# Performance work log

Hardware: AMD Instinct MI355X
Metric: run time of the kernel (lower is better)

Reference implementation:

```python
import jax, jax.numpy as jnp
import numpy as np

B, N, NINP, NFEAT, H = 4096, 4096, 64, 32, 4


def setup_inputs() -> dict:
    key = jax.random.key(0)
    ks = jax.random.split(key, 8)
    s_in = 1.0 / np.sqrt(NINP)
    s_att = 1.0 / np.sqrt(2 * NFEAT)
    return {
        "X": jax.random.normal(ks[0], (B, NINP), jnp.float32),
        "G": jax.random.normal(ks[1], (N, NINP), jnp.float32),
        "A": jax.random.uniform(ks[2], (B, N), jnp.float32),  # additive mask
        "W": jax.random.uniform(ks[3], (H, NINP, NFEAT), jnp.float32, -s_in, s_in),
        "b": jax.random.uniform(ks[4], (H, NFEAT), jnp.float32, -s_in, s_in),
        "a_src": jax.random.uniform(ks[5], (H, NFEAT), jnp.float32, -s_att, s_att),
        "a_dst": jax.random.uniform(ks[6], (H, NFEAT), jnp.float32, -s_att, s_att),
        "att_b": jax.random.uniform(ks[7], (H,), jnp.float32, -s_att, s_att),
    }


def reference(X, G, A, W, b, a_src, a_dst, att_b):
    # Per-head linear transforms (all heads batched via einsum)
    WX = jnp.einsum("bi,hif->bhf", X, W) + b            # (B, H, F)
    WG = jnp.einsum("ni,hif->nhf", G, W) + b            # (N, H, F)
    # Decomposed concat-attention: a^T [WX_b ; WG_n] = a_src.WX_b + a_dst.WG_n
    s_src = jnp.einsum("bhf,hf->bh", WX, a_src)         # (B, H)
    s_dst = jnp.einsum("nhf,hf->nh", WG, a_dst)         # (N, H)
    e = s_src[:, :, None] + s_dst.T[None, :, :] + att_b[None, :, None]  # (B,H,N)
    att = jax.nn.softmax(e - A[:, None, :], axis=-1)    # adjacency-masked softmax
    # Dropout(0.5) is identity in eval mode (deterministic reference).
    out = jnp.einsum("bhn,nhf->bhf", att, WG)           # weighted aggregation
    out = jax.nn.relu(out)                              # activation before concat
    return out.reshape(out.shape[0], -1)                # (B, H*F) concat heads
```

## Files before the change

### kernel.cpp

```cpp
#include <hip/hip_runtime.h>
#include <stdint.h>

#define N_TOK 4096
#define D_IN  64
#define NF    32
#define NH    4
#define OUTW  (NH * NF)
#define NT    8
#define CHUNK 128
#define BT    64

typedef float        f32x4  __attribute__((ext_vector_type(4)));
typedef unsigned int uint4v __attribute__((ext_vector_type(4)));
typedef __bf16       bf16x8 __attribute__((ext_vector_type(8)));

union Frag { uint4v u; bf16x8 v; };

static __device__ __forceinline__ unsigned short f2bf_rne(float x) {
  unsigned u = __float_as_uint(x);
  u += 0x7fffu + ((u >> 16) & 1u);
  return (unsigned short)(u >> 16);
}

__global__ __launch_bounds__(128) void prep_kernel(
    const float* __restrict__ G, const float* __restrict__ W,
    const float* __restrict__ bias, const float* __restrict__ a_dst,
    unsigned short* __restrict__ PB) {
  __shared__ float gs[NT * D_IN];
  const int tid = threadIdx.x;
  const int n0  = blockIdx.x * NT;
  {
    const float4* src = (const float4*)(G + (size_t)n0 * D_IN);
    float4* dst = (float4*)gs;
    dst[tid] = src[tid];
  }
  __syncthreads();
  const int h = tid >> 5, f = tid & 31;
  float acc[NT];
  const float bb = bias[h * NF + f];
#pragma unroll
  for (int k = 0; k < NT; ++k) acc[k] = bb;
#pragma unroll
  for (int i = 0; i < D_IN; ++i) {
    const float wv = W[(h * D_IN + i) * NF + f];
#pragma unroll
    for (int k = 0; k < NT; ++k) acc[k] = fmaf(gs[k * D_IN + i], wv, acc[k]);
  }
  const float ad = a_dst[h * NF + f];
  float ev[NT];
#pragma unroll
  for (int k = 0; k < NT; ++k) {
    float s = acc[k] * ad;
    s += __shfl_xor(s, 1);  s += __shfl_xor(s, 2);  s += __shfl_xor(s, 4);
    s += __shfl_xor(s, 8);  s += __shfl_xor(s, 16);
    ev[k] = __expf(s);
  }
  const int t   = n0 >> 5;
  const int gq  = (n0 >> 3) & 3;
  const int set = (h << 1) | (f >> 4);
  const int col = f & 15;
  union { uint4 u4; unsigned short us[8]; } pk;
#pragma unroll
  for (int k = 0; k < NT; ++k) pk.us[k] = f2bf_rne(acc[k] * ev[k]);
  *(uint4*)(PB + (size_t)((((t * 9 + set) << 6) + (gq << 4) + col)) * 8) = pk.u4;
  if (f == 0) {
    union { uint4 u4; unsigned short us[8]; } pe;
#pragma unroll
    for (int k = 0; k < NT; ++k) pe.us[k] = f2bf_rne(ev[k]);
    *(uint4*)(PB + (size_t)((((t * 9 + 8) << 6) + (gq << 4) + h)) * 8) = pe.u4;
  }
  if (h == 0 && f >= 4 && f < 16) {
    uint4 z; z.x = 0u; z.y = 0u; z.z = 0u; z.w = 0u;
    *(uint4*)(PB + (size_t)((((t * 9 + 8) << 6) + (gq << 4) + f)) * 8) = z;
  }
}

template <int NS>
__global__ __launch_bounds__(512) void attn_kernel(
    const float* __restrict__ A, const unsigned short* __restrict__ PB,
    float* __restrict__ op, float* __restrict__ dp, float* __restrict__ out) {
  constexpr int NHALF  = N_TOK / NS;
  constexpr int NIT    = NHALF / CHUNK;
  constexpr int RINGSZ = BT * CHUNK * 2;
  __shared__ __align__(16) unsigned short ring[3 * BT * CHUNK];
  __shared__ float denLds[BT * NH];
  char* ringb = (char*)ring;

  const int tid  = threadIdx.x;
  const int lane = tid & 63;
  const int w    = tid >> 6;
  const int bid  = blockIdx.x;
  const int s    = bid & (NS - 1);
  const int b0   = (bid / NS) * BT;

  const int srow = tid >> 3, tp = tid & 7;
  const float* abase = A + (size_t)(b0 + srow) * N_TOK + s * NHALF + tp * 16;
  const int wb0 = srow * 256 + (((tp * 2    ) ^ (srow & 15)) << 4);
  const int wb1 = srow * 256 + (((tp * 2 + 1) ^ (srow & 15)) << 4);

  const int rowm = lane & 15, g = lane >> 4;
  const char* pbb  = (const char*)PB + (size_t)s * (NHALF / 32) * 9216;
  const char* pown = pbb + (((w << 6) + lane) << 4);
  const char* pden = pbb + (((8 << 6) + lane) << 4);

  f32x4 acc0  = {0.f, 0.f, 0.f, 0.f}, acc1  = {0.f, 0.f, 0.f, 0.f};
  f32x4 acc2  = {0.f, 0.f, 0.f, 0.f}, acc3  = {0.f, 0.f, 0.f, 0.f};
  f32x4 accd0 = {0.f, 0.f, 0.f, 0.f}, accd1 = {0.f, 0.f, 0.f, 0.f};
  f32x4 accd2 = {0.f, 0.f, 0.f, 0.f}, accd3 = {0.f, 0.f, 0.f, 0.f};
  f32x4 aXa, aXb, aXc, aXd, aYa, aYb, aYc, aYd;
  Frag bo0, bo1, bo2, bo3, bd0, bd1, bd2, bd3;
  Frag co0, co1, co2, co3, cd0, cd1, cd2, cd3;
  int mR = 0, mW = 1;

#define LOADA4(d0, d1, d2, d3, cc) do {                                        \
    const float* ap_ = abase + (size_t)(cc) * CHUNK;                           \
    asm volatile("global_load_dwordx4 %0, %1, off"                            \
                 : "=v"(d0) : "v"(ap_) : "memory");                            \
    asm volatile("global_load_dwordx4 %0, %1, off"                            \
                 : "=v"(d1) : "v"(ap_ + 4) : "memory");                        \
    asm volatile("global_load_dwordx4 %0, %1, off"                            \
                 : "=v"(d2) : "v"(ap_ + 8) : "memory");                        \
    asm volatile("global_load_dwordx4 %0, %1, off"                            \
                 : "=v"(d3) : "v"(ap_ + 12) : "memory");                       \
  } while (0)
#define LOADBO(fr, cc, kk)                                                     \
  asm volatile("global_load_dwordx4 %0, %1, off"                              \
               : "=v"(fr.u)                                                    \
               : "v"(pown + (size_t)((cc) * 4 + (kk)) * 9216) : "memory")
#define LOADBD(fr, cc, kk)                                                     \
  asm volatile("global_load_dwordx4 %0, %1, off"                              \
               : "=v"(fr.u)                                                    \
               : "v"(pden + (size_t)((cc) * 4 + (kk)) * 9216) : "memory")

#define EXPP(AV0, AV1, AV2, AV3, mw) do {                                      \
    float x0 = __expf(-AV0[0]), x1 = __expf(-AV0[1]);                          \
    float x2 = __expf(-AV0[2]), x3 = __expf(-AV0[3]);                          \
    float x4 = __expf(-AV1[0]), x5 = __expf(-AV1[1]);                          \
    float x6 = __expf(-AV1[2]), x7 = __expf(-AV1[3]);                          \
    float y0 = __expf(-AV2[0]), y1 = __expf(-AV2[1]);                          \
    float y2 = __expf(-AV2[2]), y3 = __expf(-AV2[3]);                          \
    float y4 = __expf(-AV3[0]), y5 = __expf(-AV3[1]);                          \
    float y6 = __expf(-AV3[2]), y7 = __expf(-AV3[3]);                          \
    uint4v t_, u_;                                                             \
    t_[0] = __builtin_amdgcn_perm(__float_as_uint(x1), __float_as_uint(x0), 0x07060302u); \
    t_[1] = __builtin_amdgcn_perm(__float_as_uint(x3), __float_as_uint(x2), 0x07060302u); \
    t_[2] = __builtin_amdgcn_perm(__float_as_uint(x5), __float_as_uint(x4), 0x07060302u); \
    t_[3] = __builtin_amdgcn_perm(__float_as_uint(x7), __float_as_uint(x6), 0x07060302u); \
    u_[0] = __builtin_amdgcn_perm(__float_as_uint(y1), __float_as_uint(y0), 0x07060302u); \
    u_[1] = __builtin_amdgcn_perm(__float_as_uint(y3), __float_as_uint(y2), 0x07060302u); \
    u_[2] = __builtin_amdgcn_perm(__float_as_uint(y5), __float_as_uint(y4), 0x07060302u); \
    u_[3] = __builtin_amdgcn_perm(__float_as_uint(y7), __float_as_uint(y6), 0x07060302u); \
    char* rb_ = ringb + (mw) * RINGSZ;                                         \
    *(uint4v*)(rb_ + wb0) = t_;                                                \
    *(uint4v*)(rb_ + wb1) = u_;                                                \
  } while (0)

#define AF(rg, kk)                                                             \
  (*(const bf16x8*)(ringb + mR * RINGSZ + ((rg) * 16 + rowm) * 256 +           \
                    ((((kk) * 4 + g) ^ rowm) << 4)))
#define MQD(ACC, ACCD, rg, kk, FB, FD) do {                                    \
    Frag af_; af_.v = AF(rg, kk);                                              \
    ACC  = __builtin_amdgcn_mfma_f32_16x16x32_bf16(af_.v, FB.v, ACC,  0, 0, 0);\
    ACCD = __builtin_amdgcn_mfma_f32_16x16x32_bf16(af_.v, FD.v, ACCD, 0, 0, 0);\
  } while (0)
#define MQO(ACC, rg, kk, FB) do {                                              \
    Frag af_; af_.v = AF(rg, kk);                                              \
    ACC = __builtin_amdgcn_mfma_f32_16x16x32_bf16(af_.v, FB.v, ACC, 0, 0, 0);  \
  } while (0)

#define ITERD(cc, AC0, AC1, AC2, AC3, AN0, AN1, AN2, AN3,                      \
              CO0, CO1, CO2, CO3, CD0, CD1, CD2, CD3,                          \
              NO0, NO1, NO2, NO3, ND0, ND1, ND2, ND3) do {                     \
    { const int cb_ = ((cc) + 1 < NIT) ? (cc) + 1 : NIT - 1;                   \
      LOADBO(NO0, cb_, 0); LOADBO(NO1, cb_, 1);                                \
      LOADBO(NO2, cb_, 2); LOADBO(NO3, cb_, 3);                                \
      LOADBD(ND0, cb_, 0); LOADBD(ND1, cb_, 1);                                \
      LOADBD(ND2, cb_, 2); LOADBD(ND3, cb_, 3); }                              \
    { const int ca_ = ((cc) + 2 < NIT) ? (cc) + 2 : NIT - 1;                   \
      LOADA4(AN0, AN1, AN2, AN3, ca_); }                                       \
    asm volatile("s_waitcnt vmcnt(12)" ::: "memory");                          \
    __builtin_amdgcn_sched_barrier(0);                                         \
    EXPP(AC0, AC1, AC2, AC3, mW);                                              \
    asm volatile("s_waitcnt lgkmcnt(0)" ::: "memory");                         \
    __builtin_amdgcn_sched_barrier(0);                                         \
    __builtin_amdgcn_s_barrier();                                              \
    MQD(acc0, accd0, 0, 0, CO0, CD0); MQD(acc1, accd1, 1, 0, CO0, CD0);        \
    MQD(acc2, accd2, 2, 0, CO0, CD0); MQD(acc3, accd3, 3, 0, CO0, CD0);        \
    MQD(acc0, accd0, 0, 1, CO1, CD1); MQD(acc1, accd1, 1, 1, CO1, CD1);        \
    MQD(acc2, accd2, 2, 1, CO1, CD1); MQD(acc3, accd3, 3, 1, CO1, CD1);        \
    MQD(acc0, accd0, 0, 2, CO2, CD2); MQD(acc1, accd1, 1, 2, CO2, CD2);        \
    MQD(acc2, accd2, 2, 2, CO2, CD2); MQD(acc3, accd3, 3, 2, CO2, CD2);        \
    MQD(acc0, accd0, 0, 3, CO3, CD3); MQD(acc1, accd1, 1, 3, CO3, CD3);        \
    MQD(acc2, accd2, 2, 3, CO3, CD3); MQD(acc3, accd3, 3, 3, CO3, CD3);        \
    mR = mW; mW = (mW + 1 == 3) ? 0 : mW + 1;                                  \
  } while (0)
#define ITERO(cc, AC0, AC1, AC2, AC3, AN0, AN1, AN2, AN3,                      \
              CO0, CO1, CO2, CO3, NO0, NO1, NO2, NO3) do {                     \
    { const int cb_ = ((cc) + 1 < NIT) ? (cc) + 1 : NIT - 1;                   \
      LOADBO(NO0, cb_, 0); LOADBO(NO1, cb_, 1);                                \
      LOADBO(NO2, cb_, 2); LOADBO(NO3, cb_, 3); }                              \
    { const int ca_ = ((cc) + 2 < NIT) ? (cc) + 2 : NIT - 1;                   \
      LOADA4(AN0, AN1, AN2, AN3, ca_); }                                       \
    asm volatile("s_waitcnt vmcnt(8)" ::: "memory");                           \
    __builtin_amdgcn_sched_barrier(0);                                         \
    EXPP(AC0, AC1, AC2, AC3, mW);                                              \
    asm volatile("s_waitcnt lgkmcnt(0)" ::: "memory");                         \
    __builtin_amdgcn_sched_barrier(0);                                         \
    __builtin_amdgcn_s_barrier();                                              \
    MQO(acc0, 0, 0, CO0); MQO(acc1, 1, 0, CO0);                                \
    MQO(acc2, 2, 0, CO0); MQO(acc3, 3, 0, CO0);                                \
    MQO(acc0, 0, 1, CO1); MQO(acc1, 1, 1, CO1);                                \
    MQO(acc2, 2, 1, CO1); MQO(acc3, 3, 1, CO1);                                \
    MQO(acc0, 0, 2, CO2); MQO(acc1, 1, 2, CO2);                                \
    MQO(acc2, 2, 2, CO2); MQO(acc3, 3, 2, CO2);                                \
    MQO(acc0, 0, 3, CO3); MQO(acc1, 1, 3, CO3);                                \
    MQO(acc2, 2, 3, CO3); MQO(acc3, 3, 3, CO3);                                \
    mR = mW; mW = (mW + 1 == 3) ? 0 : mW + 1;                                  \
  } while (0)

  if (w == 0) {
    LOADA4(aXa, aXb, aXc, aXd, 0);
    LOADBO(bo0, 0, 0); LOADBO(bo1, 0, 1); LOADBO(bo2, 0, 2); LOADBO(bo3, 0, 3);
    LOADBD(bd0, 0, 0); LOADBD(bd1, 0, 1); LOADBD(bd2, 0, 2); LOADBD(bd3, 0, 3);
    LOADA4(aYa, aYb, aYc, aYd, 1);
    asm volatile("s_waitcnt vmcnt(12)" ::: "memory");
    __builtin_amdgcn_sched_barrier(0);
    EXPP(aXa, aXb, aXc, aXd, 0);
#pragma unroll 1
    for (int i = 0; i < NIT; i += 2) {
      ITERD(i,     aYa, aYb, aYc, aYd, aXa, aXb, aXc, aXd,
                   bo0, bo1, bo2, bo3, bd0, bd1, bd2, bd3,
                   co0, co1, co2, co3, cd0, cd1, cd2, cd3);
      ITERD(i + 1, aXa, aXb, aXc, aXd, aYa, aYb, aYc, aYd,
                   co0, co1, co2, co3, cd0, cd1, cd2, cd3,
                   bo0, bo1, bo2, bo3, bd0, bd1, bd2, bd3);
    }
  } else {
    LOADA4(aXa, aXb, aXc, aXd, 0);
    LOADBO(bo0, 0, 0); LOADBO(bo1, 0, 1); LOADBO(bo2, 0, 2); LOADBO(bo3, 0, 3);
    LOADA4(aYa, aYb, aYc, aYd, 1);
    asm volatile("s_waitcnt vmcnt(8)" ::: "memory");
    __builtin_amdgcn_sched_barrier(0);
    EXPP(aXa, aXb, aXc, aXd, 0);
#pragma unroll 1
    for (int i = 0; i < NIT; i += 2) {
      ITERO(i,     aYa, aYb, aYc, aYd, aXa, aXb, aXc, aXd,
                   bo0, bo1, bo2, bo3, co0, co1, co2, co3);
      ITERO(i + 1, aXa, aXb, aXc, aXd, aYa, aYb, aYc, aYd,
                   co0, co1, co2, co3, bo0, bo1, bo2, bo3);
    }
  }

  asm volatile("s_waitcnt vmcnt(0)" ::: "memory");
  __builtin_amdgcn_sched_barrier(0);

  if (NS == 1) {
    if (w == 0 && rowm < NH) {
#pragma unroll
      for (int r = 0; r < 4; ++r) {
        denLds[(     g * 4 + r) * NH + rowm] = accd0[r];
        denLds[(16 + g * 4 + r) * NH + rowm] = accd1[r];
        denLds[(32 + g * 4 + r) * NH + rowm] = accd2[r];
        denLds[(48 + g * 4 + r) * NH + rowm] = accd3[r];
      }
    }
    __syncthreads();
    const int hh = w >> 1;
#pragma unroll
    for (int r = 0; r < 4; ++r) {
      const int rr = g * 4 + r;
      float o;
      o = acc0[r] / denLds[(     rr) * NH + hh];
      out[(size_t)(b0 +      rr) * OUTW + w * 16 + rowm] = o > 0.f ? o : 0.f;
      o = acc1[r] / denLds[(16 + rr) * NH + hh];
      out[(size_t)(b0 + 16 + rr) * OUTW + w * 16 + rowm] = o > 0.f ? o : 0.f;
      o = acc2[r] / denLds[(32 + rr) * NH + hh];
      out[(size_t)(b0 + 32 + rr) * OUTW + w * 16 + rowm] = o > 0.f ? o : 0.f;
      o = acc3[r] / denLds[(48 + rr) * NH + hh];
      out[(size_t)(b0 + 48 + rr) * OUTW + w * 16 + rowm] = o > 0.f ? o : 0.f;
    }
  } else {
    float* ob = op + (size_t)s * (N_TOK * OUTW) + (size_t)b0 * OUTW + w * 16 + rowm;
#pragma unroll
    for (int r = 0; r < 4; ++r) {
      const int rr = g * 4 + r;
      ob[(size_t)(     rr) * OUTW] = acc0[r];
      ob[(size_t)(16 + rr) * OUTW] = acc1[r];
      ob[(size_t)(32 + rr) * OUTW] = acc2[r];
      ob[(size_t)(48 + rr) * OUTW] = acc3[r];
    }
    if (w == 0 && rowm < NH) {
#pragma unroll
      for (int r = 0; r < 4; ++r) {
        const int rr = g * 4 + r;
        dp[((size_t)s * N_TOK + b0 +      rr) * NH + rowm] = accd0[r];
        dp[((size_t)s * N_TOK + b0 + 16 + rr) * NH + rowm] = accd1[r];
        dp[((size_t)s * N_TOK + b0 + 32 + rr) * NH + rowm] = accd2[r];
        dp[((size_t)s * N_TOK + b0 + 48 + rr) * NH + rowm] = accd3[r];
      }
    }
  }
#undef LOADA4
#undef LOADBO
#undef LOADBD
#undef EXPP
#undef AF
#undef MQD
#undef MQO
#undef ITERD
#undef ITERO
}

__global__ __launch_bounds__(256) void comb_kernel(
    const float* __restrict__ op, const float* __restrict__ dp,
    float* __restrict__ out, int NS) {
  const int idx4 = blockIdx.x * 256 + threadIdx.x;
  const int eb = idx4 >> 5;
  const int h  = ((idx4 << 2) & 127) >> 5;
  float4 o; o.x = 0.f; o.y = 0.f; o.z = 0.f; o.w = 0.f;
  float d = 0.f;
  for (int s2 = 0; s2 < NS; ++s2) {
    float4 vv = *(const float4*)(op + (size_t)s2 * (N_TOK * OUTW) + (size_t)idx4 * 4);
    o.x += vv.x; o.y += vv.y; o.z += vv.z; o.w += vv.w;
    d += dp[((size_t)s2 * N_TOK + eb) * NH + h];
  }
  const float r = 1.f / d;
  float4 res;
  res.x = fmaxf(o.x * r, 0.f);
  res.y = fmaxf(o.y * r, 0.f);
  res.z = fmaxf(o.z * r, 0.f);
  res.w = fmaxf(o.w * r, 0.f);
  *(float4*)(out + (size_t)idx4 * 4) = res;
}

extern "C" void kernel_launch(void* const* d_in, const int* in_sizes, int n_in,
                              void* d_out, int out_size, void* d_ws, size_t ws_size,
                              hipStream_t stream) {
  const float* G     = (const float*)d_in[1];
  const float* A     = (const float*)d_in[2];
  const float* W     = (const float*)d_in[3];
  const float* bias  = (const float*)d_in[4];
  const float* a_dst = (const float*)d_in[6];

  char* ws = (char*)d_ws;
  const size_t PBsz = (size_t)128 * 9 * 1024;
  const size_t per_split = (size_t)N_TOK * OUTW * 4 + (size_t)N_TOK * NH * 4;

  unsigned short* PB = (unsigned short*)ws;
  float* op = (float*)(ws + PBsz);
  float* outp = (float*)d_out;

  prep_kernel<<<N_TOK / NT, 128, 0, stream>>>(G, W, bias, a_dst, PB);
  if (ws_size >= PBsz + 4 * per_split) {
    float* dp = (float*)(ws + PBsz + 4 * (size_t)N_TOK * OUTW * 4);
    attn_kernel<4><<<(N_TOK / BT) * 4, 512, 0, stream>>>(A, PB, op, dp, nullptr);
    comb_kernel<<<(N_TOK * OUTW / 4) / 256, 256, 0, stream>>>(op, dp, outp, 4);
  } else if (ws_size >= PBsz + 2 * per_split) {
    float* dp = (float*)(ws + PBsz + 2 * (size_t)N_TOK * OUTW * 4);
    attn_kernel<2><<<(N_TOK / BT) * 2, 512, 0, stream>>>(A, PB, op, dp, nullptr);
    comb_kernel<<<(N_TOK * OUTW / 4) / 256, 256, 0, stream>>>(op, dp, outp, 2);
  } else {
    attn_kernel<1><<<N_TOK / BT, 512, 0, stream>>>(A, PB, nullptr, nullptr, outp);
  }
}
```

Before: 32.49 us.

## Add 8-way key split and load denominator B fragments just-in-time

Adds an 8-way split of the key dimension when the workspace is large enough, launching twice as many attention blocks and combining eight partial results afterwards. Wave 0's denominator fragments are no longer double-buffered one chunk ahead; they are loaded at the start of each iteration and waited on just before the MFMAs. This frees registers and adds parallelism for the 64-block-per-split grid, at the cost of extra partial-result traffic in the combine step and less latency hiding for the denominator loads.

```diff
diff --git a/kernel.cpp b/kernel.cpp
--- a/kernel.cpp
+++ b/kernel.cpp
@@ -108,8 +108,9 @@
   f32x4 accd0 = {0.f, 0.f, 0.f, 0.f}, accd1 = {0.f, 0.f, 0.f, 0.f};
   f32x4 accd2 = {0.f, 0.f, 0.f, 0.f}, accd3 = {0.f, 0.f, 0.f, 0.f};
   f32x4 aXa, aXb, aXc, aXd, aYa, aYb, aYc, aYd;
-  Frag bo0, bo1, bo2, bo3, bd0, bd1, bd2, bd3;
-  Frag co0, co1, co2, co3, cd0, cd1, cd2, cd3;
+  Frag bo0, bo1, bo2, bo3;
+  Frag co0, co1, co2, co3;
+  Frag bd0, bd1, bd2, bd3;
   int mR = 0, mW = 1;
 
 #define LOADA4(d0, d1, d2, d3, cc) do {                                        \
@@ -169,13 +170,12 @@
   } while (0)
 
 #define ITERD(cc, AC0, AC1, AC2, AC3, AN0, AN1, AN2, AN3,                      \
-              CO0, CO1, CO2, CO3, CD0, CD1, CD2, CD3,                          \
-              NO0, NO1, NO2, NO3, ND0, ND1, ND2, ND3) do {                     \
+              CO0, CO1, CO2, CO3, NO0, NO1, NO2, NO3) do {                     \
+    LOADBD(bd0, cc, 0); LOADBD(bd1, cc, 1);                                    \
+    LOADBD(bd2, cc, 2); LOADBD(bd3, cc, 3);                                    \
     { const int cb_ = ((cc) + 1 < NIT) ? (cc) + 1 : NIT - 1;                   \
       LOADBO(NO0, cb_, 0); LOADBO(NO1, cb_, 1);                                \
-      LOADBO(NO2, cb_, 2); LOADBO(NO3, cb_, 3);                                \
-      LOADBD(ND0, cb_, 0); LOADBD(ND1, cb_, 1);                                \
-      LOADBD(ND2, cb_, 2); LOADBD(ND3, cb_, 3); }                              \
+      LOADBO(NO2, cb_, 2); LOADBO(NO3, cb_, 3); }                              \
     { const int ca_ = ((cc) + 2 < NIT) ? (cc) + 2 : NIT - 1;                   \
       LOADA4(AN0, AN1, AN2, AN3, ca_); }                                       \
     asm volatile("s_waitcnt vmcnt(12)" ::: "memory");                          \
@@ -184,14 +184,16 @@
     asm volatile("s_waitcnt lgkmcnt(0)" ::: "memory");                         \
     __builtin_amdgcn_sched_barrier(0);                                         \
     __builtin_amdgcn_s_barrier();                                              \
-    MQD(acc0, accd0, 0, 0, CO0, CD0); MQD(acc1, accd1, 1, 0, CO0, CD0);        \
-    MQD(acc2, accd2, 2, 0, CO0, CD0); MQD(acc3, accd3, 3, 0, CO0, CD0);        \
-    MQD(acc0, accd0, 0, 1, CO1, CD1); MQD(acc1, accd1, 1, 1, CO1, CD1);        \
-    MQD(acc2, accd2, 2, 1, CO1, CD1); MQD(acc3, accd3, 3, 1, CO1, CD1);        \
-    MQD(acc0, accd0, 0, 2, CO2, CD2); MQD(acc1, accd1, 1, 2, CO2, CD2);        \
-    MQD(acc2, accd2, 2, 2, CO2, CD2); MQD(acc3, accd3, 3, 2, CO2, CD2);        \
-    MQD(acc0, accd0, 0, 3, CO3, CD3); MQD(acc1, accd1, 1, 3, CO3, CD3);        \
-    MQD(acc2, accd2, 2, 3, CO3, CD3); MQD(acc3, accd3, 3, 3, CO3, CD3);        \
+    asm volatile("s_waitcnt vmcnt(8)" ::: "memory");                           \
+    __builtin_amdgcn_sched_barrier(0);                                         \
+    MQD(acc0, accd0, 0, 0, CO0, bd0); MQD(acc1, accd1, 1, 0, CO0, bd0);        \
+    MQD(acc2, accd2, 2, 0, CO0, bd0); MQD(acc3, accd3, 3, 0, CO0, bd0);        \
+    MQD(acc0, accd0, 0, 1, CO1, bd1); MQD(acc1, accd1, 1, 1, CO1, bd1);        \
+    MQD(acc2, accd2, 2, 1, CO1, bd1); MQD(acc3, accd3, 3, 1, CO1, bd1);        \
+    MQD(acc0, accd0, 0, 2, CO2, bd2); MQD(acc1, accd1, 1, 2, CO2, bd2);        \
+    MQD(acc2, accd2, 2, 2, CO2, bd2); MQD(acc3, accd3, 3, 2, CO2, bd2);        \
+    MQD(acc0, accd0, 0, 3, CO3, bd3); MQD(acc1, accd1, 1, 3, CO3, bd3);        \
+    MQD(acc2, accd2, 2, 3, CO3, bd3); MQD(acc3, accd3, 3, 3, CO3, bd3);        \
     mR = mW; mW = (mW + 1 == 3) ? 0 : mW + 1;                                  \
   } while (0)
 #define ITERO(cc, AC0, AC1, AC2, AC3, AN0, AN1, AN2, AN3,                      \
@@ -221,19 +223,16 @@
   if (w == 0) {
     LOADA4(aXa, aXb, aXc, aXd, 0);
     LOADBO(bo0, 0, 0); LOADBO(bo1, 0, 1); LOADBO(bo2, 0, 2); LOADBO(bo3, 0, 3);
-    LOADBD(bd0, 0, 0); LOADBD(bd1, 0, 1); LOADBD(bd2, 0, 2); LOADBD(bd3, 0, 3);
     LOADA4(aYa, aYb, aYc, aYd, 1);
-    asm volatile("s_waitcnt vmcnt(12)" ::: "memory");
+    asm volatile("s_waitcnt vmcnt(8)" ::: "memory");
     __builtin_amdgcn_sched_barrier(0);
     EXPP(aXa, aXb, aXc, aXd, 0);
 #pragma unroll 1
     for (int i = 0; i < NIT; i += 2) {
       ITERD(i,     aYa, aYb, aYc, aYd, aXa, aXb, aXc, aXd,
-                   bo0, bo1, bo2, bo3, bd0, bd1, bd2, bd3,
-                   co0, co1, co2, co3, cd0, cd1, cd2, cd3);
+                   bo0, bo1, bo2, bo3, co0, co1, co2, co3);
       ITERD(i + 1, aXa, aXb, aXc, aXd, aYa, aYb, aYc, aYd,
-                   co0, co1, co2, co3, cd0, cd1, cd2, cd3,
-                   bo0, bo1, bo2, bo3, bd0, bd1, bd2, bd3);
+                   co0, co1, co2, co3, bo0, bo1, bo2, bo3);
     }
   } else {
     LOADA4(aXa, aXb, aXc, aXd, 0);
@@ -351,7 +350,11 @@
   float* outp = (float*)d_out;
 
   prep_kernel<<<N_TOK / NT, 128, 0, stream>>>(G, W, bias, a_dst, PB);
-  if (ws_size >= PBsz + 4 * per_split) {
+  if (ws_size >= PBsz + 8 * per_split) {
+    float* dp = (float*)(ws + PBsz + 8 * (size_t)N_TOK * OUTW * 4);
+    attn_kernel<8><<<(N_TOK / BT) * 8, 512, 0, stream>>>(A, PB, op, dp, nullptr);
+    comb_kernel<<<(N_TOK * OUTW / 4) / 256, 256, 0, stream>>>(op, dp, outp, 8);
+  } else if (ws_size >= PBsz + 4 * per_split) {
     float* dp = (float*)(ws + PBsz + 4 * (size_t)N_TOK * OUTW * 4);
     attn_kernel<4><<<(N_TOK / BT) * 4, 512, 0, stream>>>(A, PB, op, dp, nullptr);
     comb_kernel<<<(N_TOK * OUTW / 4) / 256, 256, 0, stream>>>(op, dp, outp, 4);
```

Result: slower. 34.20 us (+5.2%).
